# Kernel optimization log

Measured on AMD Instinct MI355X. Metric: run time of the kernel, lower is better.

The kernel has to match this reference:

```python
import jax, jax.numpy as jnp
import numpy as np

N_NODES = 100000
N_EDGES = 1600000
D_IN = 128
D_HID = 128
N_CLS = 64
EPS = 1e-12  # torch F.normalize default eps


def setup_inputs() -> dict:
    key = jax.random.key(0)
    ks = jax.random.split(key, 8)
    x = jax.random.normal(ks[0], (N_NODES, D_IN), dtype=jnp.float32)
    src = jax.random.randint(ks[1], (N_EDGES,), 0, N_NODES, dtype=jnp.int32)
    dst = jax.random.randint(ks[2], (N_EDGES,), 0, N_NODES, dtype=jnp.int32)
    edge_weight = jax.random.uniform(ks[3], (N_EDGES,), dtype=jnp.float32)
    W1 = jax.random.normal(ks[4], (D_IN, D_HID), dtype=jnp.float32) * (1.0 / np.sqrt(D_IN))
    b1 = jnp.zeros((D_HID,), dtype=jnp.float32)
    W2 = jax.random.normal(ks[5], (D_HID, N_CLS), dtype=jnp.float32) * (1.0 / np.sqrt(D_HID))
    b2 = jnp.zeros((N_CLS,), dtype=jnp.float32)
    return {"x": x, "src": src, "dst": dst, "edge_weight": edge_weight,
            "W1": W1, "b1": b1, "W2": W2, "b2": b2}


def _spmm(h, src, dst, w):
    # sparse adjacency aggregation: out[i] = sum_{e: dst[e]==i} w[e] * h[src[e]]
    msgs = h[src] * w[:, None]  # [E, D] gather + scale
    return jax.ops.segment_sum(msgs, dst, num_segments=N_NODES)


def reference(x, src, dst, edge_weight, W1, b1, W2, b2):
    # F.normalize: row-wise L2 normalization
    norm = jnp.sqrt(jnp.sum(x * x, axis=1, keepdims=True))
    xn = x / jnp.maximum(norm, EPS)
    # GCN layer 1: A @ (X W1 + b1), ReLU (dropout is identity in eval)
    h = xn @ W1 + b1
    h = jax.nn.relu(_spmm(h, src, dst, edge_weight))
    # GCN layer 2: A @ (H W2 + b2)
    h2 = _spmm(h @ W2 + b2, src, dst, edge_weight)
    # final softmax over classes
    return jax.nn.softmax(h2, axis=-1)
```

## Files before the change

kernel.cpp:

```cpp
#include <hip/hip_runtime.h>
#include <math.h>

constexpr int NN = 100000;
constexpr int NE = 1600000;
constexpr int DI = 128;
constexpr int DH = 128;
constexpr int NC = 64;
constexpr int NB = (NN + 255) / 256;

__device__ __forceinline__ unsigned short f2bf(float f) {
    const unsigned u = __float_as_uint(f);
    return (unsigned short)((u + 0x7FFFu + ((u >> 16) & 1u)) >> 16);
}
__device__ __forceinline__ float bf_lo(unsigned u) {
    return __uint_as_float(u << 16);
}
__device__ __forceinline__ float bf_hi(unsigned u) {
    return __uint_as_float(u & 0xFFFF0000u);
}
constexpr float INV_WQ = 1.0f / 32767.0f;

__global__ __launch_bounds__(512) void k_norm_gemm1(
    const float* __restrict__ x, const float* __restrict__ W1,
    const float* __restrict__ b1, unsigned short* __restrict__ z1h)
{
    __shared__ float4 sW4[64][64];
    __shared__ float sx[8][4][DI];

    const int tid = threadIdx.x;
    for (int i = tid; i < 64 * 64; i += 512) {
        const int k2 = i >> 6, c = i & 63;
        const float* wp = W1 + (size_t)(2 * k2) * DH + c;
        sW4[k2][c] = make_float4(wp[0], wp[64], wp[DH], wp[DH + 64]);
    }
    __syncthreads();

    const int wave = tid >> 6, lane = tid & 63;
    const float bias0 = b1[lane];
    const float bias1 = b1[64 + lane];

    for (int base = (blockIdx.x * 8 + wave) * 4; base < NN;
         base += gridDim.x * 32) {
        #pragma unroll
        for (int r = 0; r < 4; ++r) {
            const int row = base + r;
            float a0 = 0.f, a1 = 0.f;
            if (row < NN) {
                a0 = x[(size_t)row * DI + lane];
                a1 = x[(size_t)row * DI + 64 + lane];
            }
            float ss = a0 * a0 + a1 * a1;
            #pragma unroll
            for (int off = 32; off; off >>= 1) ss += __shfl_xor(ss, off);
            const float rinv = 1.0f / fmaxf(sqrtf(ss), 1e-12f);
            sx[wave][r][lane]      = a0 * rinv;
            sx[wave][r][64 + lane] = a1 * rinv;
        }

        float acc[4][2];
        #pragma unroll
        for (int r = 0; r < 4; ++r) { acc[r][0] = bias0; acc[r][1] = bias1; }

        #pragma unroll 2
        for (int k2 = 0; k2 < 64; k2 += 2) {
            const float4 w0 = sW4[k2][lane];
            const float4 w1 = sW4[k2 + 1][lane];
            #pragma unroll
            for (int r = 0; r < 4; ++r) {
                const float4 xv = *(const float4*)(&sx[wave][r][2 * k2]);
                acc[r][0] = fmaf(xv.x, w0.x, acc[r][0]);
                acc[r][1] = fmaf(xv.x, w0.y, acc[r][1]);
                acc[r][0] = fmaf(xv.y, w0.z, acc[r][0]);
                acc[r][1] = fmaf(xv.y, w0.w, acc[r][1]);
                acc[r][0] = fmaf(xv.z, w1.x, acc[r][0]);
                acc[r][1] = fmaf(xv.z, w1.y, acc[r][1]);
                acc[r][0] = fmaf(xv.w, w1.z, acc[r][0]);
                acc[r][1] = fmaf(xv.w, w1.w, acc[r][1]);
            }
        }
        #pragma unroll
        for (int r = 0; r < 4; ++r) {
            const int row = base + r;
            if (row < NN) {
                z1h[(size_t)row * DH + lane]      = f2bf(acc[r][0]);
                z1h[(size_t)row * DH + 64 + lane] = f2bf(acc[r][1]);
            }
        }
    }
}

__global__ __launch_bounds__(256) void k_packW2q(
    const float* __restrict__ W2, float4* __restrict__ W2q)
{
    const int i = blockIdx.x * 256 + threadIdx.x;
    const int k4 = i >> 6, c = i & 63;
    W2q[i] = make_float4(W2[(size_t)(4 * k4 + 0) * NC + c],
                         W2[(size_t)(4 * k4 + 1) * NC + c],
                         W2[(size_t)(4 * k4 + 2) * NC + c],
                         W2[(size_t)(4 * k4 + 3) * NC + c]);
}

__global__ __launch_bounds__(256) void k_hist(
    const int* __restrict__ dst, int* __restrict__ cnt,
    int* __restrict__ rank)
{
    for (int e = blockIdx.x * 256 + threadIdx.x; e < NE; e += gridDim.x * 256)
        rank[e] = atomicAdd(&cnt[dst[e]], 1);
}

__global__ __launch_bounds__(256) void k_scanA(
    const int* __restrict__ cnt, int* __restrict__ rowptr,
    int* __restrict__ bsum)
{
    __shared__ int tmp[256];
    const int t = threadIdx.x;
    const int gid = blockIdx.x * 256 + t;
    const int v = (gid < NN) ? cnt[gid] : 0;
    tmp[t] = v;
    __syncthreads();
    #pragma unroll
    for (int off = 1; off < 256; off <<= 1) {
        const int add = (t >= off) ? tmp[t - off] : 0;
        __syncthreads();
        tmp[t] += add;
        __syncthreads();
    }
    if (gid < NN) rowptr[gid] = tmp[t] - v;
    if (t == 255) bsum[blockIdx.x] = tmp[255];
}

__global__ __launch_bounds__(512) void k_scanB(int* __restrict__ bsum)
{
    __shared__ int tmp[512];
    const int t = threadIdx.x;
    const int v = (t < NB) ? bsum[t] : 0;
    tmp[t] = v;
    __syncthreads();
    #pragma unroll
    for (int off = 1; off < 512; off <<= 1) {
        const int add = (t >= off) ? tmp[t - off] : 0;
        __syncthreads();
        tmp[t] += add;
        __syncthreads();
    }
    if (t < NB) bsum[t] = tmp[t] - v;
}

__global__ __launch_bounds__(256) void k_scanC(
    int* __restrict__ rowptr, const int* __restrict__ bsum)
{
    const int gid = blockIdx.x * 256 + threadIdx.x;
    if (gid < NN) rowptr[gid] += bsum[blockIdx.x];
    if (gid == 0) rowptr[NN] = NE;
}

__global__ __launch_bounds__(256) void k_scatter(
    const int* __restrict__ src, const int* __restrict__ dst,
    const float* __restrict__ ew, const int* __restrict__ rowptr,
    const int* __restrict__ rank, unsigned* __restrict__ srcw)
{
    for (int e = blockIdx.x * 256 + threadIdx.x; e < NE; e += gridDim.x * 256) {
        const int pos = rowptr[dst[e]] + rank[e];
        const unsigned wq = (unsigned)__float2int_rn(ew[e] * 32767.f);
        srcw[pos] = (((unsigned)src[e]) << 15) | wq;
    }
}

__global__ __launch_bounds__(512, 4) void k_spmm1_gemm2(
    const unsigned short* __restrict__ h, const int* __restrict__ rowptr,
    const unsigned* __restrict__ srcw, const float4* __restrict__ W2q,
    const float* __restrict__ b2, unsigned short* __restrict__ z2h)
{
    __shared__ float4 sW2q[32 * 64];
    __shared__ float sagg[8][DH];

    const int tid = threadIdx.x;
    #pragma unroll
    for (int i = 0; i < 4; ++i)
        sW2q[tid + i * 512] = W2q[tid + i * 512];
    __syncthreads();

    const int wave = tid >> 6, lane = tid & 63;
    const float bias = b2[lane];
    const unsigned* hu = (const unsigned*)h;

    for (int row = blockIdx.x * 8 + wave; row < NN; row += gridDim.x * 8) {
        const int start = rowptr[row], end = rowptr[row + 1];
        float acc0 = 0.f, acc1 = 0.f;
        int e = start;
        for (; e + 8 <= end; e += 8) {
            const unsigned p0 = srcw[e + 0], p1 = srcw[e + 1];
            const unsigned p2 = srcw[e + 2], p3 = srcw[e + 3];
            const unsigned p4 = srcw[e + 4], p5 = srcw[e + 5];
            const unsigned p6 = srcw[e + 6], p7 = srcw[e + 7];
            const unsigned u0 = hu[((p0 >> 15) << 6) | lane];
            const unsigned u1 = hu[((p1 >> 15) << 6) | lane];
            const unsigned u2 = hu[((p2 >> 15) << 6) | lane];
            const unsigned u3 = hu[((p3 >> 15) << 6) | lane];
            const unsigned u4 = hu[((p4 >> 15) << 6) | lane];
            const unsigned u5 = hu[((p5 >> 15) << 6) | lane];
            const unsigned u6 = hu[((p6 >> 15) << 6) | lane];
            const unsigned u7 = hu[((p7 >> 15) << 6) | lane];
            const float w0 = (float)(p0 & 0x7FFFu) * INV_WQ;
            const float w1 = (float)(p1 & 0x7FFFu) * INV_WQ;
            const float w2 = (float)(p2 & 0x7FFFu) * INV_WQ;
            const float w3 = (float)(p3 & 0x7FFFu) * INV_WQ;
            const float w4 = (float)(p4 & 0x7FFFu) * INV_WQ;
            const float w5 = (float)(p5 & 0x7FFFu) * INV_WQ;
            const float w6 = (float)(p6 & 0x7FFFu) * INV_WQ;
            const float w7 = (float)(p7 & 0x7FFFu) * INV_WQ;
            acc0 = fmaf(w0, bf_lo(u0), acc0); acc1 = fmaf(w0, bf_hi(u0), acc1);
            acc0 = fmaf(w1, bf_lo(u1), acc0); acc1 = fmaf(w1, bf_hi(u1), acc1);
            acc0 = fmaf(w2, bf_lo(u2), acc0); acc1 = fmaf(w2, bf_hi(u2), acc1);
            acc0 = fmaf(w3, bf_lo(u3), acc0); acc1 = fmaf(w3, bf_hi(u3), acc1);
            acc0 = fmaf(w4, bf_lo(u4), acc0); acc1 = fmaf(w4, bf_hi(u4), acc1);
            acc0 = fmaf(w5, bf_lo(u5), acc0); acc1 = fmaf(w5, bf_hi(u5), acc1);
            acc0 = fmaf(w6, bf_lo(u6), acc0); acc1 = fmaf(w6, bf_hi(u6), acc1);
            acc0 = fmaf(w7, bf_lo(u7), acc0); acc1 = fmaf(w7, bf_hi(u7), acc1);
        }
        for (; e < end; ++e) {
            const unsigned p = srcw[e];
            const unsigned u = hu[((p >> 15) << 6) | lane];
            const float w = (float)(p & 0x7FFFu) * INV_WQ;
            acc0 = fmaf(w, bf_lo(u), acc0);
            acc1 = fmaf(w, bf_hi(u), acc1);
        }
        *(float2*)&sagg[wave][2 * lane] =
            make_float2(fmaxf(acc0, 0.f), fmaxf(acc1, 0.f));

        float acc = bias;
        #pragma unroll 4
        for (int k4 = 0; k4 < 32; ++k4) {
            const float4 w = sW2q[k4 * 64 + lane];
            const float4 a = *(const float4*)(&sagg[wave][4 * k4]);
            acc = fmaf(a.x, w.x, acc);
            acc = fmaf(a.y, w.y, acc);
            acc = fmaf(a.z, w.z, acc);
            acc = fmaf(a.w, w.w, acc);
        }
        z2h[(size_t)row * NC + lane] = f2bf(acc);
    }
}

__global__ __launch_bounds__(256, 8) void k_spmm2_softmax(
    const unsigned short* __restrict__ z2h, const int* __restrict__ rowptr,
    const unsigned* __restrict__ srcw, float* __restrict__ out)
{
    const int row = blockIdx.x * 4 + (threadIdx.x >> 6);
    if (row >= NN) return;
    const int lane = threadIdx.x & 63;
    const int start = rowptr[row], end = rowptr[row + 1];
    float acc = 0.f;
    int e = start;
    for (; e + 8 <= end; e += 8) {
        const unsigned p0 = srcw[e + 0], p1 = srcw[e + 1];
        const unsigned p2 = srcw[e + 2], p3 = srcw[e + 3];
        const unsigned p4 = srcw[e + 4], p5 = srcw[e + 5];
        const unsigned p6 = srcw[e + 6], p7 = srcw[e + 7];
        const unsigned short t0 = z2h[((p0 >> 15) << 6) | lane];
        const unsigned short t1 = z2h[((p1 >> 15) << 6) | lane];
        const unsigned short t2 = z2h[((p2 >> 15) << 6) | lane];
        const unsigned short t3 = z2h[((p3 >> 15) << 6) | lane];
        const unsigned short t4 = z2h[((p4 >> 15) << 6) | lane];
        const unsigned short t5 = z2h[((p5 >> 15) << 6) | lane];
        const unsigned short t6 = z2h[((p6 >> 15) << 6) | lane];
        const unsigned short t7 = z2h[((p7 >> 15) << 6) | lane];
        acc = fmaf((float)(p0 & 0x7FFFu) * INV_WQ,
                   __uint_as_float((unsigned)t0 << 16), acc);
        acc = fmaf((float)(p1 & 0x7FFFu) * INV_WQ,
                   __uint_as_float((unsigned)t1 << 16), acc);
        acc = fmaf((float)(p2 & 0x7FFFu) * INV_WQ,
                   __uint_as_float((unsigned)t2 << 16), acc);
        acc = fmaf((float)(p3 & 0x7FFFu) * INV_WQ,
                   __uint_as_float((unsigned)t3 << 16), acc);
        acc = fmaf((float)(p4 & 0x7FFFu) * INV_WQ,
                   __uint_as_float((unsigned)t4 << 16), acc);
        acc = fmaf((float)(p5 & 0x7FFFu) * INV_WQ,
                   __uint_as_float((unsigned)t5 << 16), acc);
        acc = fmaf((float)(p6 & 0x7FFFu) * INV_WQ,
                   __uint_as_float((unsigned)t6 << 16), acc);
        acc = fmaf((float)(p7 & 0x7FFFu) * INV_WQ,
                   __uint_as_float((unsigned)t7 << 16), acc);
    }
    for (; e < end; ++e) {
        const unsigned p = srcw[e];
        const float v = __uint_as_float(
            (unsigned)z2h[((p >> 15) << 6) | lane] << 16);
        acc = fmaf((float)(p & 0x7FFFu) * INV_WQ, v, acc);
    }
    float m = acc;
    #pragma unroll
    for (int off = 32; off; off >>= 1) m = fmaxf(m, __shfl_xor(m, off));
    const float ex = __expf(acc - m);
    float s = ex;
    #pragma unroll
    for (int off = 32; off; off >>= 1) s += __shfl_xor(s, off);
    out[(size_t)row * NC + lane] = ex / s;
}

extern "C" void kernel_launch(void* const* d_in, const int* in_sizes, int n_in,
                              void* d_out, int out_size, void* d_ws,
                              size_t ws_size, hipStream_t stream)
{
    const float* x  = (const float*)d_in[0];
    const int* src  = (const int*)d_in[1];
    const int* dst  = (const int*)d_in[2];
    const float* ew = (const float*)d_in[3];
    const float* W1 = (const float*)d_in[4];
    const float* b1 = (const float*)d_in[5];
    const float* W2 = (const float*)d_in[6];
    const float* b2 = (const float*)d_in[7];
    float* out = (float*)d_out;

    char* base = (char*)d_ws;
    unsigned short* z1h = (unsigned short*)base;  base += (size_t)NN * DH * 2;
    unsigned short* z2h = (unsigned short*)base;  base += (size_t)NN * NC * 2;
    unsigned* srcw = (unsigned*)base;             base += (size_t)NE * 4;
    int* rank   = (int*)base;                     base += (size_t)NE * 4;
    int* rowptr = (int*)base;                     base += ((size_t)NN + 2) * 4;
    int* cnt    = (int*)base;                     base += (size_t)NN * 4;
    int* bsum   = (int*)base;                     base += 512 * 4;
    float4* W2q = (float4*)base;                  base += 2048 * 16;

    hipMemsetAsync(cnt, 0, (size_t)NN * 4, stream);

    k_packW2q<<<8, 256, 0, stream>>>(W2, W2q);
    k_norm_gemm1<<<1024, 512, 0, stream>>>(x, W1, b1, z1h);

    k_hist   <<<2048, 256, 0, stream>>>(dst, cnt, rank);
    k_scanA  <<<NB, 256, 0, stream>>>(cnt, rowptr, bsum);
    k_scanB  <<<1, 512, 0, stream>>>(bsum);
    k_scanC  <<<NB, 256, 0, stream>>>(rowptr, bsum);
    k_scatter<<<2048, 256, 0, stream>>>(src, dst, ew, rowptr, rank, srcw);

    k_spmm1_gemm2   <<<2048, 512, 0, stream>>>(z1h, rowptr, srcw, W2q, b2, z2h);
    k_spmm2_softmax <<<(NN + 3) / 4, 256, 0, stream>>>(z2h, rowptr, srcw, out);
}
```

Baseline: 320.9 us.

## Fuse GEMM1 with degree histogram in one launch and deepen SpMM gather unrolling

Merges the normalize+GEMM1 kernel and the dst histogram kernel into a single launch, with extra blocks dedicated to the atomic histogram so both independent stages run concurrently. GEMM1 now splits output columns across block pairs (64 columns each) with 2 rows per wave, which lowers per-block LDS and registers but recomputes the row normalization twice. Both SpMM kernels add a 16-edge unrolled gather loop to put more loads in flight. The fused kernel also sets a launch-bounds occupancy hint.

After: 353.4 us. +10.1%, slower.

```diff
diff --git a/kernel.cpp b/kernel.cpp
--- a/kernel.cpp
+++ b/kernel.cpp
@@ -7,6 +7,8 @@
 constexpr int DH = 128;
 constexpr int NC = 64;
 constexpr int NB = (NN + 255) / 256;
+constexpr int GB = 2048;
+constexpr int HB = 1024;
 
 __device__ __forceinline__ unsigned short f2bf(float f) {
     const unsigned u = __float_as_uint(f);
@@ -20,29 +22,40 @@
 }
 constexpr float INV_WQ = 1.0f / 32767.0f;
 
-__global__ __launch_bounds__(512) void k_norm_gemm1(
+__global__ __launch_bounds__(512, 4) void k_gemm1_hist(
     const float* __restrict__ x, const float* __restrict__ W1,
-    const float* __restrict__ b1, unsigned short* __restrict__ z1h)
-{
-    __shared__ float4 sW4[64][64];
-    __shared__ float sx[8][4][DI];
+    const float* __restrict__ b1, unsigned short* __restrict__ z1h,
+    const int* __restrict__ dst, int* __restrict__ cnt,
+    int* __restrict__ rank)
+{
+    __shared__ float4 sWq[32 * 64];
+    __shared__ float sx[8][2][DI];
 
     const int tid = threadIdx.x;
-    for (int i = tid; i < 64 * 64; i += 512) {
-        const int k2 = i >> 6, c = i & 63;
-        const float* wp = W1 + (size_t)(2 * k2) * DH + c;
-        sW4[k2][c] = make_float4(wp[0], wp[64], wp[DH], wp[DH + 64]);
+    const int bid = blockIdx.x;
+
+    if (bid >= GB) {
+        const int hb = bid - GB;
+        for (int e = hb * 512 + tid; e < NE; e += HB * 512)
+            rank[e] = atomicAdd(&cnt[dst[e]], 1);
+        return;
+    }
+
+    const int c0 = (bid & 1) * 64;
+    const int chunk = bid >> 1;
+    for (int i = tid; i < 32 * 64; i += 512) {
+        const int k4 = i >> 6, c = i & 63;
+        const float* wp = W1 + (size_t)(4 * k4) * DH + c0 + c;
+        sWq[i] = make_float4(wp[0], wp[DH], wp[2 * DH], wp[3 * DH]);
     }
     __syncthreads();
 
     const int wave = tid >> 6, lane = tid & 63;
-    const float bias0 = b1[lane];
-    const float bias1 = b1[64 + lane];
-
-    for (int base = (blockIdx.x * 8 + wave) * 4; base < NN;
-         base += gridDim.x * 32) {
-        #pragma unroll
-        for (int r = 0; r < 4; ++r) {
+    const float bias = b1[c0 + lane];
+
+    for (int base = (chunk * 8 + wave) * 2; base < NN; base += 16384) {
+        #pragma unroll
+        for (int r = 0; r < 2; ++r) {
             const int row = base + r;
             float a0 = 0.f, a1 = 0.f;
             if (row < NN) {
@@ -57,35 +70,21 @@
             sx[wave][r][64 + lane] = a1 * rinv;
         }
 
-        float acc[4][2];
-        #pragma unroll
-        for (int r = 0; r < 4; ++r) { acc[r][0] = bias0; acc[r][1] = bias1; }
-
-        #pragma unroll 2
-        for (int k2 = 0; k2 < 64; k2 += 2) {
-            const float4 w0 = sW4[k2][lane];
-            const float4 w1 = sW4[k2 + 1][lane];
-            #pragma unroll
-            for (int r = 0; r < 4; ++r) {
-                const float4 xv = *(const float4*)(&sx[wave][r][2 * k2]);
-                acc[r][0] = fmaf(xv.x, w0.x, acc[r][0]);
-                acc[r][1] = fmaf(xv.x, w0.y, acc[r][1]);
-                acc[r][0] = fmaf(xv.y, w0.z, acc[r][0]);
-                acc[r][1] = fmaf(xv.y, w0.w, acc[r][1]);
-                acc[r][0] = fmaf(xv.z, w1.x, acc[r][0]);
-                acc[r][1] = fmaf(xv.z, w1.y, acc[r][1]);
-                acc[r][0] = fmaf(xv.w, w1.z, acc[r][0]);
-                acc[r][1] = fmaf(xv.w, w1.w, acc[r][1]);
-            }
-        }
-        #pragma unroll
-        for (int r = 0; r < 4; ++r) {
-            const int row = base + r;
-            if (row < NN) {
-                z1h[(size_t)row * DH + lane]      = f2bf(acc[r][0]);
-                z1h[(size_t)row * DH + 64 + lane] = f2bf(acc[r][1]);
-            }
-        }
+        float acc0 = bias, acc1 = bias;
+        #pragma unroll 4
+        for (int k4 = 0; k4 < 32; ++k4) {
+            const float4 w  = sWq[k4 * 64 + lane];
+            const float4 xa = *(const float4*)(&sx[wave][0][4 * k4]);
+            const float4 xb = *(const float4*)(&sx[wave][1][4 * k4]);
+            acc0 = fmaf(xa.x, w.x, acc0); acc0 = fmaf(xa.y, w.y, acc0);
+            acc0 = fmaf(xa.z, w.z, acc0); acc0 = fmaf(xa.w, w.w, acc0);
+            acc1 = fmaf(xb.x, w.x, acc1); acc1 = fmaf(xb.y, w.y, acc1);
+            acc1 = fmaf(xb.z, w.z, acc1); acc1 = fmaf(xb.w, w.w, acc1);
+        }
+        if (base < NN)
+            z1h[(size_t)base * DH + c0 + lane] = f2bf(acc0);
+        if (base + 1 < NN)
+            z1h[(size_t)(base + 1) * DH + c0 + lane] = f2bf(acc1);
     }
 }
 
@@ -100,14 +99,6 @@
                          W2[(size_t)(4 * k4 + 3) * NC + c]);
 }
 
-__global__ __launch_bounds__(256) void k_hist(
-    const int* __restrict__ dst, int* __restrict__ cnt,
-    int* __restrict__ rank)
-{
-    for (int e = blockIdx.x * 256 + threadIdx.x; e < NE; e += gridDim.x * 256)
-        rank[e] = atomicAdd(&cnt[dst[e]], 1);
-}
-
 __global__ __launch_bounds__(256) void k_scanA(
     const int* __restrict__ cnt, int* __restrict__ rowptr,
     int* __restrict__ bsum)
@@ -188,35 +179,31 @@
         const int start = rowptr[row], end = rowptr[row + 1];
         float acc0 = 0.f, acc1 = 0.f;
         int e = start;
+        for (; e + 16 <= end; e += 16) {
+            unsigned p[16], u[16];
+            #pragma unroll
+            for (int j = 0; j < 16; ++j) p[j] = srcw[e + j];
+            #pragma unroll
+            for (int j = 0; j < 16; ++j) u[j] = hu[((p[j] >> 15) << 6) | lane];
+            #pragma unroll
+            for (int j = 0; j < 16; ++j) {
+                const float w = (float)(p[j] & 0x7FFFu) * INV_WQ;
+                acc0 = fmaf(w, bf_lo(u[j]), acc0);
+                acc1 = fmaf(w, bf_hi(u[j]), acc1);
+            }
+        }
         for (; e + 8 <= end; e += 8) {
-            const unsigned p0 = srcw[e + 0], p1 = srcw[e + 1];
-            const unsigned p2 = srcw[e + 2], p3 = srcw[e + 3];
-            const unsigned p4 = srcw[e + 4], p5 = srcw[e + 5];
-            const unsigned p6 = srcw[e + 6], p7 = srcw[e + 7];
-            const unsigned u0 = hu[((p0 >> 15) << 6) | lane];
-            const unsigned u1 = hu[((p1 >> 15) << 6) | lane];
-            const unsigned u2 = hu[((p2 >> 15) << 6) | lane];
-            const unsigned u3 = hu[((p3 >> 15) << 6) | lane];
-            const unsigned u4 = hu[((p4 >> 15) << 6) | lane];
-            const unsigned u5 = hu[((p5 >> 15) << 6) | lane];
-            const unsigned u6 = hu[((p6 >> 15) << 6) | lane];
-            const unsigned u7 = hu[((p7 >> 15) << 6) | lane];
-            const float w0 = (float)(p0 & 0x7FFFu) * INV_WQ;
-            const float w1 = (float)(p1 & 0x7FFFu) * INV_WQ;
-            const float w2 = (float)(p2 & 0x7FFFu) * INV_WQ;
-            const float w3 = (float)(p3 & 0x7FFFu) * INV_WQ;
-            const float w4 = (float)(p4 & 0x7FFFu) * INV_WQ;
-            const float w5 = (float)(p5 & 0x7FFFu) * INV_WQ;
-            const float w6 = (float)(p6 & 0x7FFFu) * INV_WQ;
-            const float w7 = (float)(p7 & 0x7FFFu) * INV_WQ;
-            acc0 = fmaf(w0, bf_lo(u0), acc0); acc1 = fmaf(w0, bf_hi(u0), acc1);
-            acc0 = fmaf(w1, bf_lo(u1), acc0); acc1 = fmaf(w1, bf_hi(u1), acc1);
-            acc0 = fmaf(w2, bf_lo(u2), acc0); acc1 = fmaf(w2, bf_hi(u2), acc1);
-            acc0 = fmaf(w3, bf_lo(u3), acc0); acc1 = fmaf(w3, bf_hi(u3), acc1);
-            acc0 = fmaf(w4, bf_lo(u4), acc0); acc1 = fmaf(w4, bf_hi(u4), acc1);
-            acc0 = fmaf(w5, bf_lo(u5), acc0); acc1 = fmaf(w5, bf_hi(u5), acc1);
-            acc0 = fmaf(w6, bf_lo(u6), acc0); acc1 = fmaf(w6, bf_hi(u6), acc1);
-            acc0 = fmaf(w7, bf_lo(u7), acc0); acc1 = fmaf(w7, bf_hi(u7), acc1);
+            unsigned p[8], u[8];
+            #pragma unroll
+            for (int j = 0; j < 8; ++j) p[j] = srcw[e + j];
+            #pragma unroll
+            for (int j = 0; j < 8; ++j) u[j] = hu[((p[j] >> 15) << 6) | lane];
+            #pragma unroll
+            for (int j = 0; j < 8; ++j) {
+                const float w = (float)(p[j] & 0x7FFFu) * INV_WQ;
+                acc0 = fmaf(w, bf_lo(u[j]), acc0);
+                acc1 = fmaf(w, bf_hi(u[j]), acc1);
+            }
         }
         for (; e < end; ++e) {
             const unsigned p = srcw[e];
@@ -252,35 +239,27 @@
     const int start = rowptr[row], end = rowptr[row + 1];
     float acc = 0.f;
     int e = start;
+    for (; e + 16 <= end; e += 16) {
+        unsigned p[16]; unsigned short t[16];
+        #pragma unroll
+        for (int j = 0; j < 16; ++j) p[j] = srcw[e + j];
+        #pragma unroll
+        for (int j = 0; j < 16; ++j) t[j] = z2h[((p[j] >> 15) << 6) | lane];
+        #pragma unroll
+        for (int j = 0; j < 16; ++j)
+            acc = fmaf((float)(p[j] & 0x7FFFu) * INV_WQ,
+                       __uint_as_float((unsigned)t[j] << 16), acc);
+    }
     for (; e + 8 <= end; e += 8) {
-        const unsigned p0 = srcw[e + 0], p1 = srcw[e + 1];
-        const unsigned p2 = srcw[e + 2], p3 = srcw[e + 3];
-        const unsigned p4 = srcw[e + 4], p5 = srcw[e + 5];
-        const unsigned p6 = srcw[e + 6], p7 = srcw[e + 7];
-        const unsigned short t0 = z2h[((p0 >> 15) << 6) | lane];
-        const unsigned short t1 = z2h[((p1 >> 15) << 6) | lane];
-        const unsigned short t2 = z2h[((p2 >> 15) << 6) | lane];
-        const unsigned short t3 = z2h[((p3 >> 15) << 6) | lane];
-        const unsigned short t4 = z2h[((p4 >> 15) << 6) | lane];
-        const unsigned short t5 = z2h[((p5 >> 15) << 6) | lane];
-        const unsigned short t6 = z2h[((p6 >> 15) << 6) | lane];
-        const unsigned short t7 = z2h[((p7 >> 15) << 6) | lane];
-        acc = fmaf((float)(p0 & 0x7FFFu) * INV_WQ,
-                   __uint_as_float((unsigned)t0 << 16), acc);
-        acc = fmaf((float)(p1 & 0x7FFFu) * INV_WQ,
-                   __uint_as_float((unsigned)t1 << 16), acc);
-        acc = fmaf((float)(p2 & 0x7FFFu) * INV_WQ,
-                   __uint_as_float((unsigned)t2 << 16), acc);
-        acc = fmaf((float)(p3 & 0x7FFFu) * INV_WQ,
-                   __uint_as_float((unsigned)t3 << 16), acc);
-        acc = fmaf((float)(p4 & 0x7FFFu) * INV_WQ,
-                   __uint_as_float((unsigned)t4 << 16), acc);
-        acc = fmaf((float)(p5 & 0x7FFFu) * INV_WQ,
-                   __uint_as_float((unsigned)t5 << 16), acc);
-        acc = fmaf((float)(p6 & 0x7FFFu) * INV_WQ,
-                   __uint_as_float((unsigned)t6 << 16), acc);
-        acc = fmaf((float)(p7 & 0x7FFFu) * INV_WQ,
-                   __uint_as_float((unsigned)t7 << 16), acc);
+        unsigned p[8]; unsigned short t[8];
+        #pragma unroll
+        for (int j = 0; j < 8; ++j) p[j] = srcw[e + j];
+        #pragma unroll
+        for (int j = 0; j < 8; ++j) t[j] = z2h[((p[j] >> 15) << 6) | lane];
+        #pragma unroll
+        for (int j = 0; j < 8; ++j)
+            acc = fmaf((float)(p[j] & 0x7FFFu) * INV_WQ,
+                       __uint_as_float((unsigned)t[j] << 16), acc);
     }
     for (; e < end; ++e) {
         const unsigned p = srcw[e];
@@ -325,9 +304,8 @@
     hipMemsetAsync(cnt, 0, (size_t)NN * 4, stream);
 
     k_packW2q<<<8, 256, 0, stream>>>(W2, W2q);
-    k_norm_gemm1<<<1024, 512, 0, stream>>>(x, W1, b1, z1h);
-
-    k_hist   <<<2048, 256, 0, stream>>>(dst, cnt, rank);
+    k_gemm1_hist<<<GB + HB, 512, 0, stream>>>(x, W1, b1, z1h, dst, cnt, rank);
+
     k_scanA  <<<NB, 256, 0, stream>>>(cnt, rowptr, bsum);
     k_scanB  <<<1, 512, 0, stream>>>(bsum);
     k_scanC  <<<NB, 256, 0, stream>>>(rowptr, bsum);
```
